# Kernel tuning notes

Hardware: AMD Instinct MI355X
Metric: run time of the kernel (lower is better)

The kernel has to match this reference:

```python
import jax, jax.numpy as jnp
import numpy as np

# irreps multiplicities: node = NSx0e + NVx1o, edge = ESx0e + EVx1o, hidden = HSx0e + HVx1o
NS, NV = 64, 32
ES, EV = 8, 8
HS, HV = 96, 32          # Gate splits HS scalars -> (HS-HV) silu scalars + HV sigmoid gates
N_NODES, N_EDGES = 10000, 100000
INV_SQRT3 = float(1.0 / np.sqrt(3.0))  # w3j(1,1,0) coefficient


def _split(x, ns, nv):
    # [N, ns + 3*nv] -> scalars [N, ns], vectors [N, nv, 3]
    return x[:, :ns], x[:, ns:].reshape(x.shape[0], nv, 3)


def _merge(s, v):
    return jnp.concatenate([s, v.reshape(v.shape[0], -1)], axis=-1)


def _fc_tp(xs, xv, ys, yv, w_ss, w_vv, w_sv, w_vs):
    """FullyConnectedTensorProduct for l<=1 irreps with path ('element') normalization.
    Paths: 0e*0e->0e, 1o*1o->0e (dot/sqrt3), 0e*1o->1o, 1o*0e->1o."""
    fan_s = w_ss.shape[0] * w_ss.shape[1] + w_vv.shape[0] * w_vv.shape[1]
    fan_v = w_sv.shape[0] * w_sv.shape[1] + w_vs.shape[0] * w_vs.shape[1]
    out_s = (jnp.einsum('eu,ev,uvw->ew', xs, ys, w_ss)
             + INV_SQRT3 * jnp.einsum('eum,evm,uvw->ew', xv, yv, w_vv)) / np.sqrt(fan_s)
    out_v = (jnp.einsum('eu,evm,uvw->ewm', xs, yv, w_sv)
             + jnp.einsum('eum,ev,uvw->ewm', xv, ys, w_vs)) / np.sqrt(fan_v)
    return out_s, out_v


def _gate(s, v, n_plain):
    # e3nn Gate: silu on plain scalars, sigmoid gates multiply each vector channel
    plain = jax.nn.silu(s[:, :n_plain])
    gates = jax.nn.sigmoid(s[:, n_plain:])
    return plain, v * gates[:, :, None]


def _lin(s, v, Ws, Wv):
    # e3nn equivariant Linear: mixes multiplicities per irrep, shared over m, 1/sqrt(fan_in)
    return (s @ Ws) / np.sqrt(Ws.shape[0]), jnp.einsum('num,uw->nwm', v, Wv) / np.sqrt(Wv.shape[0])


def setup_inputs() -> dict:
    key = jax.random.key(0)
    ks = jax.random.split(key, 15)
    rn = lambda k, sh: jax.random.normal(k, sh, dtype=jnp.float32)
    return {
        'node_features': rn(ks[0], (N_NODES, NS + 3 * NV)),
        'edge_attr': rn(ks[1], (N_EDGES, ES + 3 * EV)),
        'w_msg_ss': rn(ks[2], (NS, ES, HS)),
        'w_msg_vv': rn(ks[3], (NV, EV, HS)),
        'w_msg_sv': rn(ks[4], (NS, EV, HV)),
        'w_msg_vs': rn(ks[5], (NV, ES, HV)),
        'w_lin_msg_s': rn(ks[6], (HS - HV, HS)),
        'w_lin_msg_v': rn(ks[7], (HV, HV)),
        'w_upd_ss': rn(ks[8], (NS, HS, HS)),
        'w_upd_vv': rn(ks[9], (NV, HV, HS)),
        'w_upd_sv': rn(ks[10], (NS, HV, HV)),
        'w_upd_vs': rn(ks[11], (NV, HS, HV)),
        'w_lin_upd_s': rn(ks[12], (HS - HV, NS)),
        'w_lin_upd_v': rn(ks[13], (HV, NV)),
        'edge_index': jax.random.randint(ks[14], (2, N_EDGES), 0, N_NODES),
    }


def reference(node_features, edge_attr, w_msg_ss, w_msg_vv, w_msg_sv, w_msg_vs,
              w_lin_msg_s, w_lin_msg_v, w_upd_ss, w_upd_vv, w_upd_sv, w_upd_vs,
              w_lin_upd_s, w_lin_upd_v, edge_index):
    row, col = edge_index[0], edge_index[1]
    ns, nv = _split(node_features, NS, NV)
    es, ev = _split(edge_attr, ES, EV)

    # messages: gather -> CG tensor product -> gate -> linear
    ms, mv = _fc_tp(ns[col], nv[col], es, ev, w_msg_ss, w_msg_vv, w_msg_sv, w_msg_vs)
    ps, pv = _gate(ms, mv, HS - HV)                  # [E, HS-HV], [E, HV, 3]
    ls, lv = _lin(ps, pv, w_lin_msg_s, w_lin_msg_v)  # [E, HS],    [E, HV, 3]

    # scatter-sum aggregation onto destination nodes
    agg_s = jax.ops.segment_sum(ls, row, num_segments=N_NODES)
    agg_v = jax.ops.segment_sum(lv, row, num_segments=N_NODES)

    # node update: CG tensor product with aggregated messages -> gate -> linear -> residual
    us, uv = _fc_tp(ns, nv, agg_s, agg_v, w_upd_ss, w_upd_vv, w_upd_sv, w_upd_vs)
    gs, gv = _gate(us, uv, HS - HV)
    ds, dv = _lin(gs, gv, w_lin_upd_s, w_lin_upd_v)  # [N, NS], [N, NV, 3]
    return _merge(ns + ds, nv + dv)
```

## Files before the change

kernel.cpp:

```cpp
#include <hip/hip_runtime.h>
#include <hip/hip_bf16.h>

constexpr int kNodes = 10000;
constexpr int kEdges = 100000;

constexpr float INV_SQRT3    = 0.57735026918962576f;
constexpr float INV_SQRT768  = 0.036084391824351615f;
constexpr float INV_SQRT7168 = 0.011811389781538352f;
constexpr float INV_SQRT5120 = 0.013975424859373686f;
constexpr float INV_SQRT32   = 0.17677669529663687f;

constexpr size_t MSGW_OFF  = 0;
constexpr size_t UPDW1_OFF = 196608;
constexpr size_t UPDW2_OFF = 1572864;
constexpr size_t MLINS_OFF = 1900544;
constexpr size_t MLINV_OFF = 1912832;
constexpr size_t ULINS_OFF = 1914880;
constexpr size_t ULINV_OFF = 1923072;
constexpr size_t CNT_OFF   = 1926144;
constexpr size_t CUR_OFF   = 1967104;
constexpr size_t PERM_OFF  = 2008064;

typedef __attribute__((ext_vector_type(8))) short bf8;
typedef __attribute__((ext_vector_type(4))) float f4;
union BF { bf8 v; short s[8]; unsigned u[4]; };

__device__ __forceinline__ short f2bf(float f) {
    union { float f; unsigned u; } c; c.f = f;
    unsigned r = c.u + 0x7fffu + ((c.u >> 16) & 1u);
    return (short)(r >> 16);
}
__device__ __forceinline__ unsigned pk2(float lo, float hi) {
    union { __hip_bfloat162 h; unsigned u; } c;
    c.h = __float22bfloat162_rn(make_float2(lo, hi));
    return c.u;
}
__device__ __forceinline__ float bf2f(unsigned short s) {
    union { float f; unsigned u; } c; c.u = ((unsigned)s) << 16; return c.f;
}
__device__ __forceinline__ f4 mfma16(bf8 a, bf8 b, f4 c) {
    return __builtin_amdgcn_mfma_f32_16x16x32_bf16(a, b, c, 0, 0, 0);
}
__device__ __forceinline__ bf8 ldB(const char* p) {
    return *(const bf8*)p;
}
__device__ __forceinline__ float fsig(float x) { return 1.0f / (1.0f + __expf(-x)); }

__global__ void prep_kernel(
    const float* __restrict__ Wmss, const float* __restrict__ Wmvv,
    const float* __restrict__ Wmsv, const float* __restrict__ Wmvs,
    const float* __restrict__ Wlms, const float* __restrict__ Wlmv,
    const float* __restrict__ Wuss, const float* __restrict__ Wuvv,
    const float* __restrict__ Wusv, const float* __restrict__ Wuvs,
    const float* __restrict__ Wlus, const float* __restrict__ Wluv,
    char* __restrict__ wout)
{
    int i = blockIdx.x * 256 + threadIdx.x;
    float v;
    short* dst;
    if (i < 98304) {
        dst = (short*)(wout + MSGW_OFF) + i;
        int t = i >> 12, q = i & 4095, r = q >> 5, c = q & 31;
        int k = t * 32 + c;
        if (r < 96) {
            v = (k < 512 ? Wmss[k * 96 + r]
                         : Wmvv[(k - 512) * 96 + r] * INV_SQRT3) * INV_SQRT768;
        } else {
            int n2 = r - 96;
            if (k < 512) { int u = k & 63, vv = k >> 6; v = Wmsv[(u * 8 + vv) * 32 + n2] * INV_SQRT768; }
            else         { v = Wmvs[(k - 512) * 32 + n2] * INV_SQRT768; }
        }
    } else if (i < 786432) {
        int j = i - 98304;
        dst = (short*)(wout + UPDW1_OFF) + j;
        int t = j / 3072, q = j % 3072, r = q >> 5, c = q & 31;
        int k = t * 32 + c;
        if (k < 6144) { int u = k & 63, vv = k >> 6;
            v = Wuss[(u * 96 + vv) * 96 + r] * INV_SQRT7168; }
        else { int r2 = k - 6144; int u = r2 & 31, vv = r2 >> 5;
            v = Wuvv[(u * 32 + vv) * 96 + r] * (INV_SQRT3 * INV_SQRT7168); }
    } else if (i < 950272) {
        int j = i - 786432;
        dst = (short*)(wout + UPDW2_OFF) + j;
        int t = j >> 10, q = j & 1023, r = q >> 5, c = q & 31;
        int k = t * 32 + c;
        if (k < 2048) { int u = k & 63, vv = k >> 6;
            v = Wusv[(u * 32 + vv) * 32 + r] * INV_SQRT5120; }
        else { int r2 = k - 2048;
            v = Wuvs[r2 * 32 + r] * INV_SQRT5120; }
    } else if (i < 956416) {
        int j = i - 950272;
        dst = (short*)(wout + MLINS_OFF) + j;
        int n = j >> 6, kk = j & 63;
        v = Wlms[kk * 96 + n] * 0.125f;
    } else if (i < 957440) {
        int j = i - 956416;
        dst = (short*)(wout + MLINV_OFF) + j;
        int n = j >> 5, kk = j & 31;
        v = Wlmv[kk * 32 + n] * INV_SQRT32;
    } else if (i < 961536) {
        int j = i - 957440;
        dst = (short*)(wout + ULINS_OFF) + j;
        int n = j >> 6, kk = j & 63;
        v = Wlus[kk * 64 + n] * 0.125f;
    } else if (i < 962560) {
        int j = i - 961536;
        dst = (short*)(wout + ULINV_OFF) + j;
        int n = j >> 5, kk = j & 31;
        v = Wluv[kk * 32 + n] * INV_SQRT32;
    } else return;
    *dst = f2bf(v);
}

__global__ __launch_bounds__(256) void hist_kernel(const int* __restrict__ eidx,
                                                   int* __restrict__ cnt)
{
    int e = blockIdx.x * 256 + threadIdx.x;
    if (e < kEdges) atomicAdd(&cnt[eidx[e]], 1);
}

__global__ __launch_bounds__(256) void scan_kernel(const int* __restrict__ cnt,
                                                   int* __restrict__ cursor)
{
    __shared__ int psum[256];
    const int t = threadIdx.x, base = t * 40;
    int s = 0;
    for (int j = 0; j < 40; ++j) { int idx = base + j; if (idx < kNodes) s += cnt[idx]; }
    psum[t] = s;
    __syncthreads();
    if (t == 0) { int a = 0; for (int i = 0; i < 256; ++i) { int x = psum[i]; psum[i] = a; a += x; } }
    __syncthreads();
    int run = psum[t];
    for (int j = 0; j < 40; ++j) {
        int idx = base + j;
        if (idx < kNodes) { cursor[idx] = run; run += cnt[idx]; }
    }
}

__global__ __launch_bounds__(256) void scatter_kernel(const int* __restrict__ eidx,
                                                      int* __restrict__ cursor,
                                                      int* __restrict__ perm)
{
    int e = blockIdx.x * 256 + threadIdx.x;
    if (e < kEdges) {
        int p = atomicAdd(&cursor[eidx[e]], 1);
        perm[p] = e;
    }
}

__global__ __launch_bounds__(256, 3) void msg_kernel(
    const float* __restrict__ nf, const float* __restrict__ ea,
    const int* __restrict__ eidx, const char* __restrict__ wout,
    float* __restrict__ agg)
{
    __shared__ char pool[49792];
    unsigned short* nf_bf = (unsigned short*)pool;
    float* ea_sh  = (float*)(pool + 21504);
    short* silu_s = (short*)pool;
    short* gat    = (short*)(pool + 9216);
    short* pv_s   = (short*)(pool + 14336);
    float* aggloc = (float*)(pool + 30720);
    int*   row_sh = (int*)(pool + 49152);
    int*   rank_sh= (int*)(pool + 49408);
    int*   rrow   = (int*)(pool + 49664);
    int*   nh_sh  = (int*)(pool + 49760);

    const int t = threadIdx.x, w = t >> 6, lane = t & 63;
    const int l15 = lane & 15, lg = lane >> 4;
    const int eblk = blockIdx.x * 64;

    const char* msgW = wout + MSGW_OFF;
    const int*  perm = (const int*)(wout + PERM_OFF);

    {
        const int i = t >> 2, j = t & 3;
        const bool valid = (eblk + i) < kEdges;
        const int pe = perm[valid ? eblk + i : kEdges - 1];
        if (j == 0) row_sh[i] = eidx[pe];
        const int col = eidx[kEdges + pe];
        const float4* src = (const float4*)(nf + (size_t)col * 160);
        for (int c = j; c < 40; c += 4) {
            float4 v4 = src[c];
            *(uint2*)&nf_bf[i * 168 + c * 4] = make_uint2(pk2(v4.x, v4.y), pk2(v4.z, v4.w));
        }
        const float4* esrc = (const float4*)(ea + (size_t)pe * 32);
        const float4 z4 = make_float4(0.f, 0.f, 0.f, 0.f);
        *(float4*)&ea_sh[i * 36 + j * 8]     = valid ? esrc[j * 2]     : z4;
        *(float4*)&ea_sh[i * 36 + j * 8 + 4] = valid ? esrc[j * 2 + 1] : z4;
    }
    __syncthreads();

    f4 accS[2][3] = {}; f4 accV[2][3] = {};
    const int Ms = w >> 1, nb = (w & 1) * 3;
    float4 ey0[2], ey1[2];
    #pragma unroll
    for (int m = 0; m < 2; ++m) {
        const int es = m * 32 + Ms * 16 + l15;
        ey0[m] = *(const float4*)&ea_sh[es * 36];
        ey1[m] = *(const float4*)&ea_sh[es * 36 + 4];
    }

    for (int kt = 0; kt < 16; ++kt) {
        const char* wb = msgW + kt * 8192;
        bf8 bs[3], bv[3];
        #pragma unroll
        for (int i = 0; i < 3; ++i) {
            bs[i] = ldB(wb + ((nb + i) * 16 + l15) * 64 + lg * 16);
            bv[i] = ldB(wb + (96 + (((3 * w + i) & 1) * 16 + l15)) * 64 + lg * 16);
        }
        #pragma unroll
        for (int m = 0; m < 2; ++m) {
            const int es = m * 32 + Ms * 16 + l15;
            const int uu = kt * 4 + lg;
            const float xs = bf2f(nf_bf[es * 168 + uu]);
            BF aS;
            aS.u[0] = pk2(xs * ey0[m].x, xs * ey0[m].y);
            aS.u[1] = pk2(xs * ey0[m].z, xs * ey0[m].w);
            aS.u[2] = pk2(xs * ey1[m].x, xs * ey1[m].y);
            aS.u[3] = pk2(xs * ey1[m].z, xs * ey1[m].w);
            #pragma unroll
            for (int i = 0; i < 3; ++i) accS[m][i] = mfma16(aS.v, bs[i], accS[m][i]);

            BF aV; int prevMv = -1;
            #pragma unroll
            for (int i = 0; i < 3; ++i) {
                const int tv = 3 * w + i, Mv = tv >> 1;
                if (Mv != prevMv) {
                    prevMv = Mv;
                    const int mc = Mv >> 1, ev = m * 32 + (Mv & 1) * 16 + l15;
                    const int kp = kt * 32 + lg * 8;
                    const int vv = kp >> 6, u0 = kp & 63;
                    const float ym = ea_sh[ev * 36 + 8 + 3 * vv + mc];
                    const uint4 xq = *(const uint4*)&nf_bf[ev * 168 + u0];
                    aV.u[0] = pk2(__uint_as_float(xq.x << 16) * ym, __uint_as_float(xq.x & 0xffff0000u) * ym);
                    aV.u[1] = pk2(__uint_as_float(xq.y << 16) * ym, __uint_as_float(xq.y & 0xffff0000u) * ym);
                    aV.u[2] = pk2(__uint_as_float(xq.z << 16) * ym, __uint_as_float(xq.z & 0xffff0000u) * ym);
                    aV.u[3] = pk2(__uint_as_float(xq.w << 16) * ym, __uint_as_float(xq.w & 0xffff0000u) * ym);
                }
                accV[m][i] = mfma16(aV.v, bv[i], accV[m][i]);
            }
        }
    }
    for (int kt = 16; kt < 24; ++kt) {
        const char* wb = msgW + kt * 8192;
        bf8 bs[3], bv[3];
        #pragma unroll
        for (int i = 0; i < 3; ++i) {
            bs[i] = ldB(wb + ((nb + i) * 16 + l15) * 64 + lg * 16);
            bv[i] = ldB(wb + (96 + (((3 * w + i) & 1) * 16 + l15)) * 64 + lg * 16);
        }
        const int uu = (kt - 16) * 4 + lg;
        #pragma unroll
        for (int m = 0; m < 2; ++m) {
            const int es = m * 32 + Ms * 16 + l15;
            const float x0 = bf2f(nf_bf[es * 168 + 64 + 3 * uu]);
            const float x1 = bf2f(nf_bf[es * 168 + 64 + 3 * uu + 1]);
            const float x2 = bf2f(nf_bf[es * 168 + 64 + 3 * uu + 2]);
            float ey_[24];
            #pragma unroll
            for (int q = 0; q < 6; ++q)
                *(float4*)&ey_[q * 4] = *(const float4*)&ea_sh[es * 36 + 8 + q * 4];
            BF aS;
            #pragma unroll
            for (int j = 0; j < 4; ++j) {
                float a0 = x0 * ey_[6*j  ] + x1 * ey_[6*j+1] + x2 * ey_[6*j+2];
                float a1 = x0 * ey_[6*j+3] + x1 * ey_[6*j+4] + x2 * ey_[6*j+5];
                aS.u[j] = pk2(a0, a1);
            }
            #pragma unroll
            for (int i = 0; i < 3; ++i) accS[m][i] = mfma16(aS.v, bs[i], accS[m][i]);

            BF aV; int prevMv = -1;
            #pragma unroll
            for (int i = 0; i < 3; ++i) {
                const int tv = 3 * w + i, Mv = tv >> 1;
                if (Mv != prevMv) {
                    prevMv = Mv;
                    const int mc = Mv >> 1, ev = m * 32 + (Mv & 1) * 16 + l15;
                    const float xm = bf2f(nf_bf[ev * 168 + 64 + 3 * uu + mc]);
                    const float4 y0 = *(const float4*)&ea_sh[ev * 36];
                    const float4 y1 = *(const float4*)&ea_sh[ev * 36 + 4];
                    aV.u[0] = pk2(xm * y0.x, xm * y0.y);
                    aV.u[1] = pk2(xm * y0.z, xm * y0.w);
                    aV.u[2] = pk2(xm * y1.x, xm * y1.y);
                    aV.u[3] = pk2(xm * y1.z, xm * y1.w);
                }
                accV[m][i] = mfma16(aV.v, bv[i], accV[m][i]);
            }
        }
    }

    __syncthreads();

    #pragma unroll
    for (int m = 0; m < 2; ++m)
        #pragma unroll
        for (int i = 0; i < 3; ++i) {
            const int n = (nb + i) * 16 + l15;
            #pragma unroll
            for (int r = 0; r < 4; ++r) {
                const int em = m * 32 + Ms * 16 + lg * 4 + r;
                const float v = accS[m][i][r];
                if (n < 64) silu_s[em * 72 + n] = f2bf(v * fsig(v));
                else        gat[em * 40 + (n - 64)] = f2bf(fsig(v));
            }
        }
    for (int idx = t; idx < 24 * 192; idx += 256) aggloc[idx] = 0.f;
    if (t == 0) {
        int nh = 0, prev = -1, cur = -1;
        for (int i2 = 0; i2 < 64; ++i2) {
            const int r = row_sh[i2];
            if (r != prev) { cur = (nh < 24) ? nh : -1; if (cur >= 0) rrow[cur] = r; ++nh; prev = r; }
            rank_sh[i2] = cur;
        }
        nh_sh[0] = (nh < 24) ? nh : 24;
    }
    __syncthreads();

    #pragma unroll
    for (int m = 0; m < 2; ++m)
        #pragma unroll
        for (int i = 0; i < 3; ++i) {
            const int tv = 3 * w + i, Mv = tv >> 1, Nv = tv & 1;
            const int mc = Mv >> 1, eb = (Mv & 1) * 16;
            const int u = Nv * 16 + l15;
            #pragma unroll
            for (int r = 0; r < 4; ++r) {
                const int em = m * 32 + eb + lg * 4 + r;
                pv_s[(mc * 64 + em) * 40 + u] = f2bf(accV[m][i][r] * bf2f(gat[em * 40 + u]));
            }
        }
    __syncthreads();

    {
        const char* mls = wout + MLINS_OFF;
        f4 acc[6] = {};
        #pragma unroll
        for (int k0 = 0; k0 < 2; ++k0) {
            const int kg = k0 * 32 + lg * 8;
            #pragma unroll
            for (int i2 = 0; i2 < 6; ++i2) {
                const int tt = w * 6 + i2, Ms2 = tt & 3, Nn = tt >> 2;
                bf8 a = *(const bf8*)&silu_s[(Ms2 * 16 + l15) * 72 + kg];
                acc[i2] = mfma16(a, ldB(mls + (Nn * 16 + l15) * 128 + kg * 2), acc[i2]);
            }
        }
        #pragma unroll
        for (int i2 = 0; i2 < 6; ++i2) {
            const int tt = w * 6 + i2, Ms2 = tt & 3, Nn = tt >> 2;
            const int n = Nn * 16 + l15;
            #pragma unroll
            for (int r = 0; r < 4; ++r) {
                const int e64 = Ms2 * 16 + lg * 4 + r;
                const int ri = rank_sh[e64];
                if (ri >= 0) atomicAdd(&aggloc[ri * 192 + n], acc[i2][r]);
                else         atomicAdd(&agg[(size_t)row_sh[e64] * 192 + n], acc[i2][r]);
            }
        }
    }
    {
        const char* mlv = wout + MLINV_OFF;
        f4 acc[6] = {};
        const int kg = lg * 8;
        BF a; int prevMv = -1;
        #pragma unroll
        for (int i2 = 0; i2 < 6; ++i2) {
            const int tt = w * 6 + i2, Mv2 = tt >> 1, Nv2 = tt & 1;
            if (Mv2 != prevMv) { prevMv = Mv2; a.v = *(const bf8*)&pv_s[(Mv2 * 16 + l15) * 40 + kg]; }
            acc[i2] = mfma16(a.v, ldB(mlv + (Nv2 * 16 + l15) * 64 + kg * 2), acc[i2]);
        }
        #pragma unroll
        for (int i2 = 0; i2 < 6; ++i2) {
            const int tt = w * 6 + i2, Mv2 = tt >> 1, Nv2 = tt & 1;
            const int w2 = Nv2 * 16 + l15;
            #pragma unroll
            for (int r = 0; r < 4; ++r) {
                const int rr = Mv2 * 16 + lg * 4 + r;
                const int mc = rr >> 6, e64 = rr & 63;
                const int c = 96 + w2 * 3 + mc;
                const int ri = rank_sh[e64];
                if (ri >= 0) atomicAdd(&aggloc[ri * 192 + c], acc[i2][r]);
                else         atomicAdd(&agg[(size_t)row_sh[e64] * 192 + c], acc[i2][r]);
            }
        }
    }
    __syncthreads();

    const int nh = nh_sh[0];
    for (int idx = t; idx < nh * 192; idx += 256) {
        const int h = idx / 192, c = idx - h * 192;
        atomicAdd(&agg[(size_t)rrow[h] * 192 + c], aggloc[h * 192 + c]);
    }
}

__global__ __launch_bounds__(512, 4) void upd_kernel(
    const float* __restrict__ nf, const char* __restrict__ wout,
    float* __restrict__ agg)
{
    __shared__ float nf_sh[32 * 164];
    __shared__ float ag_sh[32 * 196];
    __shared__ float gat[32 * 36];
    __shared__ short silu_s[32 * 72];
    __shared__ short gv_s[96 * 40];
    __shared__ float red[3072];

    const int t = threadIdx.x, w = t >> 6, lane = t & 63;
    const int g = w >> 2, wl = w & 3;
    const int l15 = lane & 15, lg = lane >> 4;
    const int nblk = blockIdx.x * 32;
    const char* W1 = wout + UPDW1_OFF;
    const char* W2 = wout + UPDW2_OFF;

    {
        const int i = t >> 4, j = t & 15;
        int n = nblk + i; if (n > kNodes - 1) n = kNodes - 1;
        const float4* src = (const float4*)(nf + (size_t)n * 160);
        for (int c = j; c < 40; c += 16) *(float4*)&nf_sh[i * 164 + c * 4] = src[c];
        const float4* asrc = (const float4*)(agg + (size_t)n * 192);
        for (int c = j; c < 48; c += 16) *(float4*)&ag_sh[i * 196 + c * 4] = asrc[c];
    }
    __syncthreads();

    const int Ms = wl >> 1, nb = (wl & 1) * 3;
    const int es_ = Ms * 16 + l15;

    f4 accS[3] = {{0.f,0.f,0.f,0.f},{0.f,0.f,0.f,0.f},{0.f,0.f,0.f,0.f}};
    {
        const int kt0 = g * 112, kt1 = kt0 + 112;
        const int ktSS = kt1 < 192 ? kt1 : 192;
        int kt = kt0;
        for (; kt < ktSS; ++kt) {
            const char* wb = W1 + (size_t)kt * 6144;
            const int kp = kt * 32 + lg * 8;
            const int vv = kp >> 6, u0 = kp & 63;
            const float ys = ag_sh[es_ * 196 + vv];
            const float4 x0 = *(const float4*)&nf_sh[es_ * 164 + u0];
            const float4 x1 = *(const float4*)&nf_sh[es_ * 164 + u0 + 4];
            BF aS;
            aS.u[0] = pk2(x0.x * ys, x0.y * ys);
            aS.u[1] = pk2(x0.z * ys, x0.w * ys);
            aS.u[2] = pk2(x1.x * ys, x1.y * ys);
            aS.u[3] = pk2(x1.z * ys, x1.w * ys);
            #pragma unroll
            for (int i = 0; i < 3; ++i)
                accS[i] = mfma16(aS.v, ldB(wb + ((nb + i) * 16 + l15) * 64 + lg * 16), accS[i]);
        }
        for (; kt < kt1; ++kt) {
            const char* wb = W1 + (size_t)kt * 6144;
            const int rp = kt * 32 + lg * 8 - 6144;
            const int vv = rp >> 5, u0 = rp & 31;
            const float* xp = &nf_sh[es_ * 164 + 64 + 3 * u0];
            const float* gp = &ag_sh[es_ * 196 + 96 + 3 * vv];
            const float g0 = gp[0], g1 = gp[1], g2 = gp[2];
            BF aS;
            #pragma unroll
            for (int j = 0; j < 4; ++j) {
                float a0 = xp[6*j  ] * g0 + xp[6*j+1] * g1 + xp[6*j+2] * g2;
                float a1 = xp[6*j+3] * g0 + xp[6*j+4] * g1 + xp[6*j+5] * g2;
                aS.u[j] = pk2(a0, a1);
            }
            #pragma unroll
            for (int i = 0; i < 3; ++i)
                accS[i] = mfma16(aS.v, ldB(wb + ((nb + i) * 16 + l15) * 64 + lg * 16), accS[i]);
        }
    }

    if (g == 1) {
        #pragma unroll
        for (int i = 0; i < 3; ++i) {
            const int n = (nb + i) * 16 + l15;
            #pragma unroll
            for (int r = 0; r < 4; ++r)
                red[(Ms * 16 + lg * 4 + r) * 96 + n] = accS[i][r];
        }
    }
    __syncthreads();
    if (g == 0) {
        #pragma unroll
        for (int i = 0; i < 3; ++i) {
            const int n = (nb + i) * 16 + l15;
            #pragma unroll
            for (int r = 0; r < 4; ++r) {
                const int e = Ms * 16 + lg * 4 + r;
                const float v = accS[i][r] + red[e * 96 + n];
                if (n < 64) silu_s[e * 72 + n] = f2bf(v * fsig(v));
                else        gat[e * 36 + (n - 64)] = fsig(v);
            }
        }
    }
    __syncthreads();

    f4 accV[3] = {{0.f,0.f,0.f,0.f},{0.f,0.f,0.f,0.f},{0.f,0.f,0.f,0.f}};
    {
        const int kt0 = g * 80, kt1 = kt0 + 80;
        const int ktSV = kt1 < 64 ? kt1 : 64;
        int kt = kt0;
        for (; kt < ktSV; ++kt) {
            const char* wb = W2 + (size_t)kt * 2048;
            BF aV; int prevMv = -1;
            #pragma unroll
            for (int i = 0; i < 3; ++i) {
                const int tv = 3 * wl + i, Mv = tv >> 1, Nv = tv & 1;
                if (Mv != prevMv) {
                    prevMv = Mv;
                    const int m = Mv >> 1, ev = (Mv & 1) * 16 + l15;
                    const int kp = kt * 32 + lg * 8;
                    const int vv = kp >> 6, u0 = kp & 63;
                    const float ym = ag_sh[ev * 196 + 96 + 3 * vv + m];
                    const float4 x0 = *(const float4*)&nf_sh[ev * 164 + u0];
                    const float4 x1 = *(const float4*)&nf_sh[ev * 164 + u0 + 4];
                    aV.u[0] = pk2(x0.x * ym, x0.y * ym);
                    aV.u[1] = pk2(x0.z * ym, x0.w * ym);
                    aV.u[2] = pk2(x1.x * ym, x1.y * ym);
                    aV.u[3] = pk2(x1.z * ym, x1.w * ym);
                }
                accV[i] = mfma16(aV.v, ldB(wb + (Nv * 16 + l15) * 64 + lg * 16), accV[i]);
            }
        }
        for (; kt < kt1; ++kt) {
            const char* wb = W2 + (size_t)kt * 2048;
            BF aV; int prevMv = -1;
            #pragma unroll
            for (int i = 0; i < 3; ++i) {
                const int tv = 3 * wl + i, Mv = tv >> 1, Nv = tv & 1;
                if (Mv != prevMv) {
                    prevMv = Mv;
                    const int m = Mv >> 1, ev = (Mv & 1) * 16 + l15;
                    const int rp = kt * 32 + lg * 8 - 2048;
                    const int u = rp / 96, v0 = rp - u * 96;
                    const float xm = nf_sh[ev * 164 + 64 + 3 * u + m];
                    const float4 y0 = *(const float4*)&ag_sh[ev * 196 + v0];
                    const float4 y1 = *(const float4*)&ag_sh[ev * 196 + v0 + 4];
                    aV.u[0] = pk2(xm * y0.x, xm * y0.y);
                    aV.u[1] = pk2(xm * y0.z, xm * y0.w);
                    aV.u[2] = pk2(xm * y1.x, xm * y1.y);
                    aV.u[3] = pk2(xm * y1.z, xm * y1.w);
                }
                accV[i] = mfma16(aV.v, ldB(wb + (Nv * 16 + l15) * 64 + lg * 16), accV[i]);
            }
        }
    }

    if (g == 1) {
        #pragma unroll
        for (int i = 0; i < 3; ++i) {
            const int tv = 3 * wl + i, Mv = tv >> 1, Nv = tv & 1;
            #pragma unroll
            for (int r = 0; r < 4; ++r)
                red[(Mv * 16 + lg * 4 + r) * 32 + Nv * 16 + l15] = accV[i][r];
        }
    }
    __syncthreads();
    if (g == 0) {
        #pragma unroll
        for (int i = 0; i < 3; ++i) {
            const int tv = 3 * wl + i, Mv = tv >> 1, Nv = tv & 1;
            const int m = Mv >> 1, eb = (Mv & 1) * 16;
            const int u = Nv * 16 + l15;
            #pragma unroll
            for (int r = 0; r < 4; ++r) {
                const int e = eb + lg * 4 + r;
                const float v = accV[i][r] + red[(Mv * 16 + lg * 4 + r) * 32 + u];
                gv_s[(m * 32 + e) * 40 + u] = f2bf(v * gat[e * 36 + u]);
            }
        }
    }
    __syncthreads();

    const int nvalid = kNodes - nblk;
    if (g == 0) {
        {
            const char* uls = wout + ULINS_OFF;
            f4 acc[2] = {{0.f,0.f,0.f,0.f},{0.f,0.f,0.f,0.f}};
            const int nb2 = (wl & 1) * 2;
            #pragma unroll
            for (int k0 = 0; k0 < 2; ++k0) {
                const int kg = k0 * 32 + lg * 8;
                bf8 a = *(const bf8*)&silu_s[es_ * 72 + kg];
                #pragma unroll
                for (int i = 0; i < 2; ++i)
                    acc[i] = mfma16(a, ldB(uls + ((nb2 + i) * 16 + l15) * 128 + kg * 2), acc[i]);
            }
            #pragma unroll
            for (int i = 0; i < 2; ++i) {
                const int n = (nb2 + i) * 16 + l15;
                #pragma unroll
                for (int r = 0; r < 4; ++r) {
                    const int e = Ms * 16 + lg * 4 + r;
                    if (e < nvalid)
                        agg[(size_t)(nblk + e) * 192 + n] = nf_sh[e * 164 + n] + acc[i][r];
                }
            }
        }
        {
            const char* ulv = wout + ULINV_OFF;
            f4 acc[3] = {{0.f,0.f,0.f,0.f},{0.f,0.f,0.f,0.f},{0.f,0.f,0.f,0.f}};
            const int kg = lg * 8;
            BF a; int prevMv = -1;
            #pragma unroll
            for (int i = 0; i < 3; ++i) {
                const int tv = 3 * wl + i, Mv = tv >> 1, Nv = tv & 1;
                if (Mv != prevMv) { prevMv = Mv; a.v = *(const bf8*)&gv_s[(Mv * 16 + l15) * 40 + kg]; }
                acc[i] = mfma16(a.v, ldB(ulv + (Nv * 16 + l15) * 64 + kg * 2), acc[i]);
            }
            #pragma unroll
            for (int i = 0; i < 3; ++i) {
                const int tv = 3 * wl + i, Mv = tv >> 1, Nv = tv & 1;
                const int w2 = Nv * 16 + l15;
                #pragma unroll
                for (int r = 0; r < 4; ++r) {
                    const int rr = Mv * 16 + lg * 4 + r;
                    const int m = rr >> 5, e = rr & 31;
                    if (e < nvalid)
                        agg[(size_t)(nblk + e) * 192 + 64 + w2 * 3 + m]
                            = nf_sh[e * 164 + 64 + w2 * 3 + m] + acc[i][r];
                }
            }
        }
    }
}

__global__ __launch_bounds__(256) void copy_kernel(const float* __restrict__ agg,
                                                   float* __restrict__ out)
{
    int i = blockIdx.x * 256 + threadIdx.x;
    if (i < 400000) {
        int n = i / 40, c = i - n * 40;
        ((float4*)out)[i] = ((const float4*)agg)[n * 48 + c];
    }
}

extern "C" void kernel_launch(void* const* d_in, const int* in_sizes, int n_in,
                              void* d_out, int out_size, void* d_ws, size_t ws_size,
                              hipStream_t stream) {
    const float* nf   = (const float*)d_in[0];
    const float* ea   = (const float*)d_in[1];
    const int*   eidx = (const int*)d_in[14];
    float* agg = (float*)d_ws;
    char*  wout = (char*)d_out;

    hipMemsetAsync(agg, 0, 7680000, stream);
    hipMemsetAsync(wout + CNT_OFF, 0, 40960, stream);
    prep_kernel<<<3760, 256, 0, stream>>>(
        (const float*)d_in[2], (const float*)d_in[3], (const float*)d_in[4],
        (const float*)d_in[5], (const float*)d_in[6], (const float*)d_in[7],
        (const float*)d_in[8], (const float*)d_in[9], (const float*)d_in[10],
        (const float*)d_in[11], (const float*)d_in[12], (const float*)d_in[13], wout);
    hist_kernel<<<391, 256, 0, stream>>>(eidx, (int*)(wout + CNT_OFF));
    scan_kernel<<<1, 256, 0, stream>>>((const int*)(wout + CNT_OFF), (int*)(wout + CUR_OFF));
    scatter_kernel<<<391, 256, 0, stream>>>(eidx, (int*)(wout + CUR_OFF), (int*)(wout + PERM_OFF));
    msg_kernel<<<(kEdges + 63) / 64, 256, 0, stream>>>(nf, ea, eidx, wout, agg);
    upd_kernel<<<(kNodes + 31) / 32, 512, 0, stream>>>(nf, wout, agg);
    copy_kernel<<<1563, 256, 0, stream>>>(agg, (float*)d_out);
}
```

Before: 472.5 us.

## Drop edge sort and LDS pre-aggregation, scatter messages directly with global atomics

Removes the histogram/scan/scatter counting sort of edges by destination and the shared-memory per-row pre-aggregation in the message kernel. Messages are now atomically added straight into the global aggregation buffer in original edge order. This eliminates three small kernels, a memset and the permutation indirection, and cuts LDS use so occupancy can rise to 5 blocks. In exchange, every message element becomes a global float atomic to a random row, greatly increasing atomic traffic and contention.

```diff
diff --git a/kernel.cpp b/kernel.cpp
--- a/kernel.cpp
+++ b/kernel.cpp
@@ -17,9 +17,6 @@
 constexpr size_t MLINV_OFF = 1912832;
 constexpr size_t ULINS_OFF = 1914880;
 constexpr size_t ULINV_OFF = 1923072;
-constexpr size_t CNT_OFF   = 1926144;
-constexpr size_t CUR_OFF   = 1967104;
-constexpr size_t PERM_OFF  = 2008064;
 
 typedef __attribute__((ext_vector_type(8))) short bf8;
 typedef __attribute__((ext_vector_type(4))) float f4;
@@ -112,78 +109,38 @@
     *dst = f2bf(v);
 }
 
-__global__ __launch_bounds__(256) void hist_kernel(const int* __restrict__ eidx,
-                                                   int* __restrict__ cnt)
-{
-    int e = blockIdx.x * 256 + threadIdx.x;
-    if (e < kEdges) atomicAdd(&cnt[eidx[e]], 1);
-}
-
-__global__ __launch_bounds__(256) void scan_kernel(const int* __restrict__ cnt,
-                                                   int* __restrict__ cursor)
-{
-    __shared__ int psum[256];
-    const int t = threadIdx.x, base = t * 40;
-    int s = 0;
-    for (int j = 0; j < 40; ++j) { int idx = base + j; if (idx < kNodes) s += cnt[idx]; }
-    psum[t] = s;
-    __syncthreads();
-    if (t == 0) { int a = 0; for (int i = 0; i < 256; ++i) { int x = psum[i]; psum[i] = a; a += x; } }
-    __syncthreads();
-    int run = psum[t];
-    for (int j = 0; j < 40; ++j) {
-        int idx = base + j;
-        if (idx < kNodes) { cursor[idx] = run; run += cnt[idx]; }
-    }
-}
-
-__global__ __launch_bounds__(256) void scatter_kernel(const int* __restrict__ eidx,
-                                                      int* __restrict__ cursor,
-                                                      int* __restrict__ perm)
-{
-    int e = blockIdx.x * 256 + threadIdx.x;
-    if (e < kEdges) {
-        int p = atomicAdd(&cursor[eidx[e]], 1);
-        perm[p] = e;
-    }
-}
-
-__global__ __launch_bounds__(256, 3) void msg_kernel(
+__global__ __launch_bounds__(256, 5) void msg_kernel(
     const float* __restrict__ nf, const float* __restrict__ ea,
     const int* __restrict__ eidx, const char* __restrict__ wout,
     float* __restrict__ agg)
 {
-    __shared__ char pool[49792];
+    __shared__ char pool[31232];
     unsigned short* nf_bf = (unsigned short*)pool;
     float* ea_sh  = (float*)(pool + 21504);
+    int*   row_sh = (int*)(pool + 30720);
     short* silu_s = (short*)pool;
     short* gat    = (short*)(pool + 9216);
     short* pv_s   = (short*)(pool + 14336);
-    float* aggloc = (float*)(pool + 30720);
-    int*   row_sh = (int*)(pool + 49152);
-    int*   rank_sh= (int*)(pool + 49408);
-    int*   rrow   = (int*)(pool + 49664);
-    int*   nh_sh  = (int*)(pool + 49760);
 
     const int t = threadIdx.x, w = t >> 6, lane = t & 63;
     const int l15 = lane & 15, lg = lane >> 4;
     const int eblk = blockIdx.x * 64;
 
     const char* msgW = wout + MSGW_OFF;
-    const int*  perm = (const int*)(wout + PERM_OFF);
 
     {
         const int i = t >> 2, j = t & 3;
-        const bool valid = (eblk + i) < kEdges;
-        const int pe = perm[valid ? eblk + i : kEdges - 1];
-        if (j == 0) row_sh[i] = eidx[pe];
-        const int col = eidx[kEdges + pe];
+        const int e = eblk + i;
+        const bool valid = e < kEdges;
+        const int ee = valid ? e : kEdges - 1;
+        if (j == 0) row_sh[i] = eidx[ee];
+        const int col = eidx[kEdges + ee];
         const float4* src = (const float4*)(nf + (size_t)col * 160);
         for (int c = j; c < 40; c += 4) {
             float4 v4 = src[c];
             *(uint2*)&nf_bf[i * 168 + c * 4] = make_uint2(pk2(v4.x, v4.y), pk2(v4.z, v4.w));
         }
-        const float4* esrc = (const float4*)(ea + (size_t)pe * 32);
+        const float4* esrc = (const float4*)(ea + (size_t)ee * 32);
         const float4 z4 = make_float4(0.f, 0.f, 0.f, 0.f);
         *(float4*)&ea_sh[i * 36 + j * 8]     = valid ? esrc[j * 2]     : z4;
         *(float4*)&ea_sh[i * 36 + j * 8 + 4] = valid ? esrc[j * 2 + 1] : z4;
@@ -305,16 +262,6 @@
                 else        gat[em * 40 + (n - 64)] = f2bf(fsig(v));
             }
         }
-    for (int idx = t; idx < 24 * 192; idx += 256) aggloc[idx] = 0.f;
-    if (t == 0) {
-        int nh = 0, prev = -1, cur = -1;
-        for (int i2 = 0; i2 < 64; ++i2) {
-            const int r = row_sh[i2];
-            if (r != prev) { cur = (nh < 24) ? nh : -1; if (cur >= 0) rrow[cur] = r; ++nh; prev = r; }
-            rank_sh[i2] = cur;
-        }
-        nh_sh[0] = (nh < 24) ? nh : 24;
-    }
     __syncthreads();
 
     #pragma unroll
@@ -352,9 +299,7 @@
             #pragma unroll
             for (int r = 0; r < 4; ++r) {
                 const int e64 = Ms2 * 16 + lg * 4 + r;
-                const int ri = rank_sh[e64];
-                if (ri >= 0) atomicAdd(&aggloc[ri * 192 + n], acc[i2][r]);
-                else         atomicAdd(&agg[(size_t)row_sh[e64] * 192 + n], acc[i2][r]);
+                atomicAdd(&agg[(size_t)row_sh[e64] * 192 + n], acc[i2][r]);
             }
         }
     }
@@ -377,19 +322,9 @@
             for (int r = 0; r < 4; ++r) {
                 const int rr = Mv2 * 16 + lg * 4 + r;
                 const int mc = rr >> 6, e64 = rr & 63;
-                const int c = 96 + w2 * 3 + mc;
-                const int ri = rank_sh[e64];
-                if (ri >= 0) atomicAdd(&aggloc[ri * 192 + c], acc[i2][r]);
-                else         atomicAdd(&agg[(size_t)row_sh[e64] * 192 + c], acc[i2][r]);
-            }
-        }
-    }
-    __syncthreads();
-
-    const int nh = nh_sh[0];
-    for (int idx = t; idx < nh * 192; idx += 256) {
-        const int h = idx / 192, c = idx - h * 192;
-        atomicAdd(&agg[(size_t)rrow[h] * 192 + c], aggloc[h * 192 + c]);
+                atomicAdd(&agg[(size_t)row_sh[e64] * 192 + 96 + w2 * 3 + mc], acc[i2][r]);
+            }
+        }
     }
 }
 
@@ -640,15 +575,11 @@
     char*  wout = (char*)d_out;
 
     hipMemsetAsync(agg, 0, 7680000, stream);
-    hipMemsetAsync(wout + CNT_OFF, 0, 40960, stream);
     prep_kernel<<<3760, 256, 0, stream>>>(
         (const float*)d_in[2], (const float*)d_in[3], (const float*)d_in[4],
         (const float*)d_in[5], (const float*)d_in[6], (const float*)d_in[7],
         (const float*)d_in[8], (const float*)d_in[9], (const float*)d_in[10],
         (const float*)d_in[11], (const float*)d_in[12], (const float*)d_in[13], wout);
-    hist_kernel<<<391, 256, 0, stream>>>(eidx, (int*)(wout + CNT_OFF));
-    scan_kernel<<<1, 256, 0, stream>>>((const int*)(wout + CNT_OFF), (int*)(wout + CUR_OFF));
-    scatter_kernel<<<391, 256, 0, stream>>>(eidx, (int*)(wout + CUR_OFF), (int*)(wout + PERM_OFF));
     msg_kernel<<<(kEdges + 63) / 64, 256, 0, stream>>>(nf, ea, eidx, wout, agg);
     upd_kernel<<<(kNodes + 31) / 32, 512, 0, stream>>>(nf, wout, agg);
     copy_kernel<<<1563, 256, 0, stream>>>(agg, (float*)d_out);
```

After: 575.6 us. +21.8%, slower.
